# Kernel tuning notes

Measured on AMD Instinct MI355X. Metric: run time of the kernel, lower is better.

## Reference

```python
import jax, jax.numpy as jnp
import numpy as np
from jax import lax


def squash(s):
    # scale = |s|^2/(1+|s|^2); out = scale * s/|s| (eps-stabilized as in source)
    norm = jnp.sum(s * s, axis=-1, keepdims=True)
    return (norm / (1.0 + norm)) * (s / jnp.sqrt(norm + 1e-8))


def setup_inputs() -> dict:
    key = jax.random.key(0)
    k = jax.random.split(key, 4)
    B, H, C = 32, 64, 10
    x = jax.random.normal(k[0], (B, 3, H, H), jnp.float32)
    conv1_w = jax.random.normal(k[1], (256, 3, 9, 9), jnp.float32) * 0.06
    conv1_b = jnp.zeros((256,), jnp.float32)
    conv2_w = jax.random.normal(k[2], (256, 256, 9, 9), jnp.float32) * 0.02  # 256 = 8 caps * 32 routes
    conv2_b = jnp.zeros((256,), jnp.float32)
    route_w = jax.random.normal(k[3], (32, C, 8, 16), jnp.float32)  # [routes, classes, in_dim, out_dim]
    return {"x": x, "conv1_w": conv1_w, "conv1_b": conv1_b,
            "conv2_w": conv2_w, "conv2_b": conv2_b, "route_w": route_w}


def reference(x, conv1_w, conv1_b, conv2_w, conv2_b, route_w):
    dn = ("NCHW", "OIHW", "NCHW")
    # PrimaryCapsules: conv 3->256 k9 s1 + relu
    h = lax.conv_general_dilated(x, conv1_w, (1, 1), "VALID", dimension_numbers=dn)
    h = jax.nn.relu(h + conv1_b[None, :, None, None])
    # CapsuleLayer conv: 256 -> 8*32 k9 s2
    h = lax.conv_general_dilated(h, conv2_w, (2, 2), "VALID", dimension_numbers=dn)
    h = h + conv2_b[None, :, None, None]
    B, _, hh, ww = h.shape
    R, D = 32, 8  # num_routes, capsule dim
    # [B, R*D, h, w] -> [B, R, P, D], squash per capsule vector
    caps = h.reshape(B, R, D, hh, ww).transpose(0, 1, 3, 4, 2).reshape(B, R, hh * ww, D)
    caps = squash(caps)
    # DigitCapsules: per-route linear maps 8->16, shared over spatial positions
    u_hat = jnp.einsum("brpi,rcio->brpco", caps, route_w)  # [B, R, P, C, 16]
    C, O = u_hat.shape[3], u_hat.shape[4]
    u_hat = u_hat.reshape(B, R * hh * ww, C, O)  # [B, N, C, 16]
    b_log = jnp.zeros(u_hat.shape[:-1], u_hat.dtype)  # [B, N, C]
    num_routing = 3
    v = None
    for i in range(num_routing):
        c = jax.nn.softmax(b_log, axis=2)            # over classes (dim=2 in source)
        s = jnp.einsum("bnc,bnco->bco", c, u_hat)    # weighted sum over input caps
        v = squash(s)                                 # [B, C, 16]
        if i < num_routing - 1:
            b_log = b_log + jnp.einsum("bnco,bco->bnc", u_hat, v)  # agreement
    return v
```

## Files before the change

kernel.cpp:

```cpp
#include <hip/hip_runtime.h>
#include <hip/hip_bf16.h>
#include <stdint.h>

typedef __attribute__((ext_vector_type(8))) short short8;
typedef __attribute__((ext_vector_type(4))) float f32x4;
typedef unsigned int u32x4a __attribute__((vector_size(16)));
typedef unsigned int u32x4u __attribute__((vector_size(16), aligned(4)));

__device__ inline unsigned short f2bf(float f) {
    union { float f; uint32_t u; } v; v.f = f;
    uint32_t u = v.u;
    uint32_t r = (u + 0x7FFFu + ((u >> 16) & 1u)) >> 16;
    return (unsigned short)r;
}

__device__ inline void gl_lds16(const unsigned short* g, unsigned short* l) {
    __builtin_amdgcn_global_load_lds(
        (const uint32_t __attribute__((address_space(1)))*)(const void*)g,
        (uint32_t __attribute__((address_space(3)))*)(void*)l, 16, 0, 0);
}

__global__ void cvt_w1(const float* __restrict__ w, unsigned short* __restrict__ A1) {
    int idx = blockIdx.x * 256 + threadIdx.x;
    int row = idx >> 8, k = idx & 255;
    float v = (k < 243) ? w[row * 243 + k] : 0.f;
    A1[idx] = f2bf(v);
}

__global__ void cvt_w2(const float* __restrict__ w, unsigned short* __restrict__ A2t) {
    int idx = blockIdx.x * 256 + threadIdx.x;
    int j = idx & 7;
    int off16 = (idx >> 3) & 1023;
    int tile = idx >> 13;
    int tm = tile / 324, chunk = tile - tm * 324;
    int row = off16 >> 3, sw = off16 & 7;
    int koct = sw ^ (row & 7);
    int kk = chunk * 64 + koct * 8 + j;
    int oc = tm * 128 + row;
    int ic, ky, kx;
    if (kk < 18432) { ic = kk / 72; int rem = kk - ic * 72; ky = rem >> 3; kx = rem & 7; }
    else { int j2 = kk - 18432; ic = j2 / 9; ky = j2 - ic * 9; kx = 8; }
    A2t[idx] = f2bf(w[((oc * 256 + ic) * 9 + ky) * 9 + kx]);
}

__global__ __launch_bounds__(256) void conv1_gemm(
    const unsigned short* __restrict__ A,
    const float* __restrict__ x,
    const float* __restrict__ bias,
    unsigned short* __restrict__ h1)
{
    __shared__ __align__(16) unsigned short As[128 * 40];
    __shared__ __align__(16) unsigned short Bs[128 * 40];
    const int tid = threadIdx.x;
    const int m0 = blockIdx.y * 128;
    const int sx = (blockIdx.x & 7) * 98 + (blockIdx.x >> 3);
    const int n0 = sx * 128;
    const int lane = tid & 63;
    const int wave = tid >> 6;
    const int wy = wave & 1, wx = wave >> 1;
    const int l16 = lane & 15, q = lane >> 4;

    const int kp = tid & 15;
    const int gn = tid >> 4;
    int baseN[8];
#pragma unroll
    for (int j = 0; j < 8; ++j) {
        int n = n0 + gn * 8 + j;
        int b = n / 3136, p = n % 3136;
        int oy = p / 56, ox = p % 56;
        baseN[j] = b * 12288 + oy * 64 + ox;
    }

    f32x4 acc[4][4];
#pragma unroll
    for (int im = 0; im < 4; ++im)
#pragma unroll
        for (int in = 0; in < 4; ++in)
            acc[im][in] = (f32x4){0.f, 0.f, 0.f, 0.f};

    for (int k0 = 0; k0 < 256; k0 += 32) {
        __syncthreads();
#pragma unroll
        for (int s = 0; s < 2; ++s) {
            int slot = tid + s * 256;
            int row = slot >> 2, seg = slot & 3;
            u32x4a v = *(const u32x4a*)(A + (m0 + row) * 256 + k0 + seg * 8);
            *(u32x4a*)(&As[row * 40 + seg * 8]) = v;
        }
        int ka = k0 + 2 * kp, kb = ka + 1;
        int offa = 0, offb = 0;
        bool va = ka < 243, vb = kb < 243;
        if (va) { int c = ka / 81, t = ka % 81, ky = t / 9, kx = t % 9; offa = c * 4096 + ky * 64 + kx; }
        if (vb) { int c = kb / 81, t = kb % 81, ky = t / 9, kx = t % 9; offb = c * 4096 + ky * 64 + kx; }
#pragma unroll
        for (int j = 0; j < 8; ++j) {
            unsigned int ba = va ? (unsigned int)f2bf(x[baseN[j] + offa]) : 0u;
            unsigned int bb = vb ? (unsigned int)f2bf(x[baseN[j] + offb]) : 0u;
            *(unsigned int*)(&Bs[(gn * 8 + j) * 40 + 2 * kp]) = ba | (bb << 16);
        }
        __syncthreads();

        short8 af[4], bf[4];
#pragma unroll
        for (int im = 0; im < 4; ++im)
            af[im] = *(const short8*)(&As[(wy * 64 + im * 16 + l16) * 40 + q * 8]);
#pragma unroll
        for (int in = 0; in < 4; ++in)
            bf[in] = *(const short8*)(&Bs[(wx * 64 + in * 16 + l16) * 40 + q * 8]);
#pragma unroll
        for (int im = 0; im < 4; ++im)
#pragma unroll
            for (int in = 0; in < 4; ++in)
                acc[im][in] = __builtin_amdgcn_mfma_f32_16x16x32_bf16(af[im], bf[in], acc[im][in], 0, 0, 0);
    }

#pragma unroll
    for (int in = 0; in < 4; ++in) {
        int n = n0 + wx * 64 + in * 16 + l16;
        int b = n / 3136, p = n % 3136;
        int oy = p / 56, ox = p % 56;
#pragma unroll
        for (int im = 0; im < 4; ++im) {
#pragma unroll
            for (int r = 0; r < 4; ++r) {
                int oc = m0 + wy * 64 + im * 16 + q * 4 + r;
                float v = acc[im][in][r] + bias[oc];
                v = v > 0.f ? v : 0.f;
                h1[((b * 256 + oc) * 56 + oy) * 56 + ox] = f2bf(v);
            }
        }
    }
}

__global__ __launch_bounds__(256, 3) void conv2_gemm(
    const unsigned short* __restrict__ A2t,
    const unsigned short* __restrict__ h1,
    float* __restrict__ c2)
{
    __shared__ __align__(16) unsigned short As[2][8192];
    __shared__ __align__(16) unsigned short BsT[128 * 72];
    const int tid = threadIdx.x;
    const int sx = (blockIdx.x & 7) * 18 + (blockIdx.x >> 3);
    const int n0 = sx * 128;
    const int z = blockIdx.z;
    const int lane = tid & 63;
    const int wave = tid >> 6;
    const int wy = wave & 1, wx = wave >> 1;
    const int l16 = lane & 15, q = lane >> 4;

    int boff[4];
#pragma unroll
    for (int in = 0; in < 4; ++in) {
        int n = n0 + wx * 64 + in * 16 + l16;
        int b = n / 576, p = n % 576;
        int oy = p / 24, ox = p % 24;
        boff[in] = b * 802816 + (2 * oy) * 56 + 2 * ox;
    }
    const int tn = tid & 127, thalf = tid >> 7;
    int tbase;
    {
        int ng = n0 + tn;
        int b = ng / 576, p = ng % 576;
        int oy = p / 24, ox = p % 24;
        tbase = b * 802816 + (2 * oy) * 56 + 2 * ox + 8;
    }

    f32x4 acc[4][4];
#pragma unroll
    for (int im = 0; im < 4; ++im)
#pragma unroll
        for (int in = 0; in < 4; ++in)
            acc[im][in] = (f32x4){0.f, 0.f, 0.f, 0.f};

    const size_t tilebase = (size_t)blockIdx.y * 324 * 8192;

    auto issueA = [&](int c, int buf) {
        const unsigned short* at = A2t + tilebase + (size_t)c * 8192;
        int s0 = wave * 4;
#pragma unroll
        for (int i = 0; i < 4; ++i) {
            int sl = (s0 + i) * 64 + lane;
            gl_lds16(at + sl * 8, &As[buf][sl * 8]);
        }
    };
    auto loadBmain = [&](int c, short8 (&B)[2][4]) {
#pragma unroll
        for (int h = 0; h < 2; ++h) {
            int octk = c * 8 + h * 4 + q;
            int ic = octk / 9;
            int ky = octk - ic * 9;
            int off = ic * 3136 + ky * 56;
#pragma unroll
            for (int in = 0; in < 4; ++in) {
                u32x4u v = *(const u32x4u*)(h1 + boff[in] + off);
                B[h][in] = __builtin_bit_cast(short8, v);
            }
        }
    };
    auto computeChunk = [&](int buf, short8 (&B)[2][4]) {
#pragma unroll
        for (int h = 0; h < 2; ++h) {
            short8 af[4];
#pragma unroll
            for (int im = 0; im < 4; ++im) {
                int row = wy * 64 + im * 16 + l16;
                int koct = h * 4 + q;
                af[im] = *(const short8*)(&As[buf][(row * 8 + (koct ^ (row & 7))) * 8]);
            }
            __builtin_amdgcn_s_setprio(1);
#pragma unroll
            for (int im = 0; im < 4; ++im)
#pragma unroll
                for (int in = 0; in < 4; ++in)
                    acc[im][in] = __builtin_amdgcn_mfma_f32_16x16x32_bf16(
                        af[im], B[h][in], acc[im][in], 0, 0, 0);
            __builtin_amdgcn_s_setprio(0);
        }
    };

    short8 B0[2][4], B1[2][4];

    issueA(z, 0);
    loadBmain(z, B0);
    __asm__ volatile("s_waitcnt vmcnt(8)" ::: "memory");
    __builtin_amdgcn_s_barrier();
    __asm__ volatile("" ::: "memory");

    int c = z;
    for (int it = 0; it < 18; ++it) {
        issueA(c + 8, 1);
        loadBmain(c + 8, B1);
        __asm__ volatile("" ::: "memory");
        computeChunk(0, B0);
        __asm__ volatile("s_waitcnt vmcnt(8)" ::: "memory");
        __builtin_amdgcn_s_barrier();
        __asm__ volatile("" ::: "memory");

        if (it < 17) {
            issueA(c + 16, 0);
            loadBmain(c + 16, B0);
        } else {
            issueA(z + 288, 0);
        }
        __asm__ volatile("" ::: "memory");
        computeChunk(1, B1);
        __asm__ volatile("s_waitcnt vmcnt(8)" ::: "memory");
        __builtin_amdgcn_s_barrier();
        __asm__ volatile("" ::: "memory");
        c += 16;
    }

    int bt = 0;
    for (int ct = z + 288; ct < 324; ct += 8) {
        uint32_t bR[16];
        int base = ct * 64 + thalf * 32 - 18432;
#pragma unroll
        for (int p = 0; p < 16; ++p) {
            int j2 = base + 2 * p;
            int icA = j2 / 9, kyA = j2 - icA * 9;
            int icB = (j2 + 1) / 9, kyB = (j2 + 1) - icB * 9;
            uint32_t ba = h1[tbase + icA * 3136 + kyA * 56];
            uint32_t bb = h1[tbase + icB * 3136 + kyB * 56];
            bR[p] = ba | (bb << 16);
        }
        if (ct + 8 < 324) issueA(ct + 8, bt ^ 1);
        __syncthreads();
#pragma unroll
        for (int p = 0; p < 16; ++p)
            *(uint32_t*)(&BsT[tn * 72 + thalf * 32 + 2 * p]) = bR[p];
        __syncthreads();
#pragma unroll
        for (int h = 0; h < 2; ++h) {
            short8 af[4], bf[4];
#pragma unroll
            for (int im = 0; im < 4; ++im) {
                int row = wy * 64 + im * 16 + l16;
                int koct = h * 4 + q;
                af[im] = *(const short8*)(&As[bt][(row * 8 + (koct ^ (row & 7))) * 8]);
            }
#pragma unroll
            for (int in = 0; in < 4; ++in)
                bf[in] = *(const short8*)(&BsT[(wx * 64 + in * 16 + l16) * 72 + h * 32 + q * 8]);
#pragma unroll
            for (int im = 0; im < 4; ++im)
#pragma unroll
                for (int in = 0; in < 4; ++in)
                    acc[im][in] = __builtin_amdgcn_mfma_f32_16x16x32_bf16(
                        af[im], bf[in], acc[im][in], 0, 0, 0);
        }
        __syncthreads();
        bt ^= 1;
    }

    const int m0 = blockIdx.y * 128;
#pragma unroll
    for (int in = 0; in < 4; ++in) {
        int nn = n0 + wx * 64 + in * 16 + l16;
        int bb = nn / 576, pp = nn % 576;
#pragma unroll
        for (int im = 0; im < 4; ++im) {
#pragma unroll
            for (int r = 0; r < 4; ++r) {
                int oc = m0 + wy * 64 + im * 16 + q * 4 + r;
                atomicAdd(&c2[(bb * 256 + oc) * 576 + pp], acc[im][in][r]);
            }
        }
    }
}

__global__ void squash_caps(const float* __restrict__ c2, const float* __restrict__ bias,
                            float* __restrict__ caps) {
    int idx = blockIdx.x * 256 + threadIdx.x;
    int b = idx / 18432;
    int rp = idx % 18432;
    int r = rp / 576, p = rp % 576;
    float s[8]; float n2 = 0.f;
#pragma unroll
    for (int d = 0; d < 8; ++d) {
        s[d] = c2[(b * 256 + r * 8 + d) * 576 + p] + bias[r * 8 + d];
        n2 += s[d] * s[d];
    }
    float sc = (n2 / (1.f + n2)) / sqrtf(n2 + 1e-8f);
#pragma unroll
    for (int d = 0; d < 8; ++d)
        caps[idx * 8 + d] = sc * s[d];
}

__global__ __launch_bounds__(64) void capsum0(const float* __restrict__ caps,
                                              float* __restrict__ G) {
    int r = blockIdx.x, b = blockIdx.y;
    const float* cp = caps + (size_t)(b * 32 + r) * 4608;
    int tid = threadIdx.x;
    f32x4 s0 = (f32x4){0.f, 0.f, 0.f, 0.f}, s1 = s0;
    for (int jv = 0; jv < 9; ++jv) {
        const f32x4* qp = (const f32x4*)(cp + (jv * 64 + tid) * 8);
        s0 += qp[0]; s1 += qp[1];
    }
#pragma unroll
    for (int off = 32; off > 0; off >>= 1) {
#pragma unroll
        for (int k = 0; k < 4; ++k) {
            s0[k] += __shfl_down(s0[k], off, 64);
            s1[k] += __shfl_down(s1[k], off, 64);
        }
    }
    if (tid == 0) {
        float g[8] = {s0[0], s0[1], s0[2], s0[3], s1[0], s1[1], s1[2], s1[3]};
        float* gp = G + (size_t)((b * 32 + r) * 10) * 8;
        for (int cc = 0; cc < 10; ++cc)
#pragma unroll
            for (int ii = 0; ii < 8; ++ii) gp[cc * 8 + ii] = g[ii] * 0.1f;
    }
}

__global__ __launch_bounds__(64) void route_accum(const float* __restrict__ caps,
                                                  const float* __restrict__ W,
                                                  const float* __restrict__ V,
                                                  float* __restrict__ G) {
    int r = blockIdx.x, b = blockIdx.y;
    __shared__ float wv[80];
    __shared__ float red[80][64];
    int tid = threadIdx.x;
    for (int v = tid; v < 80; v += 64) {
        int cc = v >> 3, ii = v & 7;
        float s = 0.f;
#pragma unroll
        for (int o = 0; o < 16; ++o)
            s += W[((r * 10 + cc) * 8 + ii) * 16 + o] * V[(b * 10 + cc) * 16 + o];
        wv[v] = s;
    }
    __syncthreads();
    float g[80];
#pragma unroll
    for (int v = 0; v < 80; ++v) g[v] = 0.f;
    const float* cp = caps + (size_t)(b * 32 + r) * 4608;
    for (int j = 0; j < 9; ++j) {
        int p = j * 64 + tid;
        const f32x4* qp = (const f32x4*)(cp + p * 8);
        f32x4 c0 = qp[0], c1 = qp[1];
        float c8[8];
#pragma unroll
        for (int i = 0; i < 4; ++i) { c8[i] = c0[i]; c8[4 + i] = c1[i]; }
        float a[10]; float m = -1e30f;
#pragma unroll
        for (int cc = 0; cc < 10; ++cc) {
            float t = 0.f;
#pragma unroll
            for (int i = 0; i < 8; ++i) t += c8[i] * wv[cc * 8 + i];
            a[cc] = t; m = fmaxf(m, t);
        }
        float sum = 0.f;
#pragma unroll
        for (int cc = 0; cc < 10; ++cc) { a[cc] = __expf(a[cc] - m); sum += a[cc]; }
        float inv = 1.f / sum;
#pragma unroll
        for (int cc = 0; cc < 10; ++cc) {
            float w = a[cc] * inv;
#pragma unroll
            for (int i = 0; i < 8; ++i) g[cc * 8 + i] += w * c8[i];
        }
    }
#pragma unroll
    for (int v = 0; v < 80; ++v) red[v][tid] = g[v];
    __syncthreads();
    for (int v = tid; v < 80; v += 64) {
        float s = 0.f;
        for (int t = 0; t < 64; ++t) s += red[v][t];
        G[(b * 32 + r) * 80 + v] = s;
    }
}

__global__ __launch_bounds__(160) void sv_kernel(const float* __restrict__ G,
                                                 const float* __restrict__ W,
                                                 float* __restrict__ V,
                                                 float* __restrict__ out, int last) {
    int b = blockIdx.x;
    int c = threadIdx.x / 16, o = threadIdx.x % 16;
    __shared__ float sL[10][16];
    float s = 0.f;
    for (int r = 0; r < 32; ++r) {
        const float* g = G + ((b * 32 + r) * 10 + c) * 8;
        const float* w = W + ((r * 10 + c) * 8) * 16 + o;
#pragma unroll
        for (int i = 0; i < 8; ++i) s += g[i] * w[i * 16];
    }
    sL[c][o] = s;
    __syncthreads();
    float n2 = 0.f;
#pragma unroll
    for (int oo = 0; oo < 16; ++oo) { float t = sL[c][oo]; n2 += t * t; }
    float sc = (n2 / (1.f + n2)) / sqrtf(n2 + 1e-8f);
    float v = sc * s;
    V[(b * 10 + c) * 16 + o] += v;
    if (last) out[(b * 10 + c) * 16 + o] = v;
}

extern "C" void kernel_launch(void* const* d_in, const int* in_sizes, int n_in,
                              void* d_out, int out_size, void* d_ws, size_t ws_size,
                              hipStream_t stream) {
    const float* x  = (const float*)d_in[0];
    const float* w1 = (const float*)d_in[1];
    const float* b1 = (const float*)d_in[2];
    const float* w2 = (const float*)d_in[3];
    const float* b2 = (const float*)d_in[4];
    const float* rw = (const float*)d_in[5];

    char* ws = (char*)d_ws;
    unsigned short* A1   = (unsigned short*)(ws);
    unsigned short* A2   = (unsigned short*)(ws + 262144);
    unsigned short* h1   = (unsigned short*)(ws + 10878976);
    float*          c2   = (float*)(ws + 62259200);
    float*          caps = (float*)(ws + 81133568);
    float*          V    = (float*)(ws + 100007936);
    float*          G    = (float*)(ws + 100028416);

    hipLaunchKernelGGL(cvt_w1, dim3(256), dim3(256), 0, stream, w1, A1);
    hipLaunchKernelGGL(cvt_w2, dim3(20736), dim3(256), 0, stream, w2, A2);
    hipMemsetAsync(c2, 0, 18874368, stream);
    hipLaunchKernelGGL(conv1_gemm, dim3(784, 2), dim3(256), 0, stream, A1, x, b1, h1);
    hipLaunchKernelGGL(conv2_gemm, dim3(144, 2, 8), dim3(256), 0, stream, A2, h1, c2);
    hipLaunchKernelGGL(squash_caps, dim3(2304), dim3(256), 0, stream, c2, b2, caps);
    hipMemsetAsync(V, 0, 5120 * sizeof(float), stream);
    hipLaunchKernelGGL(capsum0, dim3(32, 32), dim3(64), 0, stream, caps, G);
    hipLaunchKernelGGL(sv_kernel, dim3(32), dim3(160), 0, stream, G, rw, V, (float*)d_out, 0);
    for (int it = 1; it < 3; ++it) {
        hipLaunchKernelGGL(route_accum, dim3(32, 32), dim3(64), 0, stream, caps, rw, V, G);
        hipLaunchKernelGGL(sv_kernel, dim3(32), dim3(160), 0, stream, G, rw, V,
                           (float*)d_out, it == 2 ? 1 : 0);
    }
}
```

Before: 457.1 us.

## Unify conv2 tail into main loop with triple-buffered A and direct B gathers

The conv2 GEMM's separate tail loop is removed. It staged scalar-gathered B values through an LDS transposed buffer with extra __syncthreads. The main loop now covers every chunk, and loadB falls back to per-element register gathers for the tail chunks. The A tile moves from double to triple buffering in LDS, so A prefetch runs two chunks ahead and waiting on the load counter is dropped in favour of a barrier. Swizzled A LDS offsets are also precomputed once. The change aims to remove tail synchronisation overhead and deepen the A prefetch, but the per-element tail gathers are many scalar loads and the loop trip count now depends on blockIdx.z.

Measured after the change: 725.4 us. 1.59x slower.

```diff
diff --git a/kernel.cpp b/kernel.cpp
--- a/kernel.cpp
+++ b/kernel.cpp
@@ -137,8 +137,7 @@
     const unsigned short* __restrict__ h1,
     float* __restrict__ c2)
 {
-    __shared__ __align__(16) unsigned short As[2][8192];
-    __shared__ __align__(16) unsigned short BsT[128 * 72];
+    __shared__ __align__(16) unsigned short As[3][8192];
     const int tid = threadIdx.x;
     const int sx = (blockIdx.x & 7) * 18 + (blockIdx.x >> 3);
     const int n0 = sx * 128;
@@ -156,14 +155,15 @@
         int oy = p / 24, ox = p % 24;
         boff[in] = b * 802816 + (2 * oy) * 56 + 2 * ox;
     }
-    const int tn = tid & 127, thalf = tid >> 7;
-    int tbase;
-    {
-        int ng = n0 + tn;
-        int b = ng / 576, p = ng % 576;
-        int oy = p / 24, ox = p % 24;
-        tbase = b * 802816 + (2 * oy) * 56 + 2 * ox + 8;
-    }
+    int aoff[2][4];
+#pragma unroll
+    for (int h = 0; h < 2; ++h)
+#pragma unroll
+        for (int im = 0; im < 4; ++im) {
+            int row = wy * 64 + im * 16 + l16;
+            int koct = h * 4 + q;
+            aoff[h][im] = (row * 8 + (koct ^ (row & 7))) * 8;
+        }
 
     f32x4 acc[4][4];
 #pragma unroll
@@ -173,40 +173,56 @@
             acc[im][in] = (f32x4){0.f, 0.f, 0.f, 0.f};
 
     const size_t tilebase = (size_t)blockIdx.y * 324 * 8192;
+    const int s0 = wave * 4;
 
     auto issueA = [&](int c, int buf) {
         const unsigned short* at = A2t + tilebase + (size_t)c * 8192;
-        int s0 = wave * 4;
 #pragma unroll
         for (int i = 0; i < 4; ++i) {
             int sl = (s0 + i) * 64 + lane;
             gl_lds16(at + sl * 8, &As[buf][sl * 8]);
         }
     };
-    auto loadBmain = [&](int c, short8 (&B)[2][4]) {
-#pragma unroll
-        for (int h = 0; h < 2; ++h) {
-            int octk = c * 8 + h * 4 + q;
-            int ic = octk / 9;
-            int ky = octk - ic * 9;
-            int off = ic * 3136 + ky * 56;
-#pragma unroll
-            for (int in = 0; in < 4; ++in) {
-                u32x4u v = *(const u32x4u*)(h1 + boff[in] + off);
-                B[h][in] = __builtin_bit_cast(short8, v);
+    auto loadB = [&](int c, short8 (&B)[2][4]) {
+        if (c < 288) {
+#pragma unroll
+            for (int h = 0; h < 2; ++h) {
+                int octk = c * 8 + h * 4 + q;
+                int ic = octk / 9;
+                int ky = octk - ic * 9;
+                int off = ic * 3136 + ky * 56;
+#pragma unroll
+                for (int in = 0; in < 4; ++in) {
+                    u32x4u v = *(const u32x4u*)(h1 + boff[in] + off);
+                    B[h][in] = __builtin_bit_cast(short8, v);
+                }
+            }
+        } else {
+#pragma unroll
+            for (int h = 0; h < 2; ++h) {
+                int kbase = c * 64 + (h * 4 + q) * 8 - 18432;
+#pragma unroll
+                for (int in = 0; in < 4; ++in) {
+                    short8 v;
+#pragma unroll
+                    for (int j = 0; j < 8; ++j) {
+                        int j2 = kbase + j;
+                        int ic = j2 / 9, ky = j2 - ic * 9;
+                        v[j] = (short)h1[boff[in] + 8 + ic * 3136 + ky * 56];
+                    }
+                    B[h][in] = v;
+                }
             }
         }
     };
     auto computeChunk = [&](int buf, short8 (&B)[2][4]) {
+        const unsigned short* ab = &As[buf][0];
 #pragma unroll
         for (int h = 0; h < 2; ++h) {
             short8 af[4];
 #pragma unroll
-            for (int im = 0; im < 4; ++im) {
-                int row = wy * 64 + im * 16 + l16;
-                int koct = h * 4 + q;
-                af[im] = *(const short8*)(&As[buf][(row * 8 + (koct ^ (row & 7))) * 8]);
-            }
+            for (int im = 0; im < 4; ++im)
+                af[im] = *(const short8*)(ab + aoff[h][im]);
             __builtin_amdgcn_s_setprio(1);
 #pragma unroll
             for (int im = 0; im < 4; ++im)
@@ -219,77 +235,42 @@
     };
 
     short8 B0[2][4], B1[2][4];
+    const int nch = (324 - z + 7) >> 3;
 
     issueA(z, 0);
-    loadBmain(z, B0);
+    issueA(z + 8, 1);
+    __asm__ volatile("" ::: "memory");
+    loadB(z, B0);
     __asm__ volatile("s_waitcnt vmcnt(8)" ::: "memory");
     __builtin_amdgcn_s_barrier();
     __asm__ volatile("" ::: "memory");
 
     int c = z;
-    for (int it = 0; it < 18; ++it) {
-        issueA(c + 8, 1);
-        loadBmain(c + 8, B1);
-        __asm__ volatile("" ::: "memory");
-        computeChunk(0, B0);
-        __asm__ volatile("s_waitcnt vmcnt(8)" ::: "memory");
+    int bufA = 0;
+    const int half = nch >> 1;
+    for (int it = 0; it < half; ++it) {
+        const int i0 = 2 * it;
+        if (i0 + 2 < nch) { int bn = bufA + 2; if (bn >= 3) bn -= 3; issueA(c + 16, bn); }
+        __asm__ volatile("" ::: "memory");
+        if (i0 + 1 < nch) loadB(c + 8, B1);
+        computeChunk(bufA, B0);
+        if (++bufA == 3) bufA = 0;
+        __asm__ volatile("" ::: "memory");
         __builtin_amdgcn_s_barrier();
         __asm__ volatile("" ::: "memory");
-
-        if (it < 17) {
-            issueA(c + 16, 0);
-            loadBmain(c + 16, B0);
-        } else {
-            issueA(z + 288, 0);
-        }
-        __asm__ volatile("" ::: "memory");
-        computeChunk(1, B1);
-        __asm__ volatile("s_waitcnt vmcnt(8)" ::: "memory");
+        c += 8;
+        if (i0 + 3 < nch) { int bn = bufA + 2; if (bn >= 3) bn -= 3; issueA(c + 16, bn); }
+        __asm__ volatile("" ::: "memory");
+        if (i0 + 2 < nch) loadB(c + 8, B0);
+        computeChunk(bufA, B1);
+        if (++bufA == 3) bufA = 0;
+        __asm__ volatile("" ::: "memory");
         __builtin_amdgcn_s_barrier();
         __asm__ volatile("" ::: "memory");
-        c += 16;
-    }
-
-    int bt = 0;
-    for (int ct = z + 288; ct < 324; ct += 8) {
-        uint32_t bR[16];
-        int base = ct * 64 + thalf * 32 - 18432;
-#pragma unroll
-        for (int p = 0; p < 16; ++p) {
-            int j2 = base + 2 * p;
-            int icA = j2 / 9, kyA = j2 - icA * 9;
-            int icB = (j2 + 1) / 9, kyB = (j2 + 1) - icB * 9;
-            uint32_t ba = h1[tbase + icA * 3136 + kyA * 56];
-            uint32_t bb = h1[tbase + icB * 3136 + kyB * 56];
-            bR[p] = ba | (bb << 16);
-        }
-        if (ct + 8 < 324) issueA(ct + 8, bt ^ 1);
-        __syncthreads();
-#pragma unroll
-        for (int p = 0; p < 16; ++p)
-            *(uint32_t*)(&BsT[tn * 72 + thalf * 32 + 2 * p]) = bR[p];
-        __syncthreads();
-#pragma unroll
-        for (int h = 0; h < 2; ++h) {
-            short8 af[4], bf[4];
-#pragma unroll
-            for (int im = 0; im < 4; ++im) {
-                int row = wy * 64 + im * 16 + l16;
-                int koct = h * 4 + q;
-                af[im] = *(const short8*)(&As[bt][(row * 8 + (koct ^ (row & 7))) * 8]);
-            }
-#pragma unroll
-            for (int in = 0; in < 4; ++in)
-                bf[in] = *(const short8*)(&BsT[(wx * 64 + in * 16 + l16) * 72 + h * 32 + q * 8]);
-#pragma unroll
-            for (int im = 0; im < 4; ++im)
-#pragma unroll
-                for (int in = 0; in < 4; ++in)
-                    acc[im][in] = __builtin_amdgcn_mfma_f32_16x16x32_bf16(
-                        af[im], bf[in], acc[im][in], 0, 0, 0);
-        }
-        __syncthreads();
-        bt ^= 1;
+        c += 8;
+    }
+    if (nch & 1) {
+        computeChunk(bufA, B0);
     }
 
     const int m0 = blockIdx.y * 128;
```

## Triple-buffer conv2 A tiles in LDS and reuse a buffer for the tail

Applied to the files above, without the earlier changes.

The main K loop of the conv2 GEMM moves from a double-buffered to a triple-buffered LDS scheme for the weight tiles. The async global-to-LDS copy is issued two chunks ahead while the activation fragments are prefetched one chunk ahead. The loop is unrolled so buffer indices are compile-time constants, and the explicit vmcnt waits give way to implicit ordering through the register-consumed B loads. The separate transposed B tile for the tail loop is dropped and stored, swizzled, into the third A buffer, which keeps LDS use about the same. Precomputed LDS fragment offsets remove per-iteration address math. The risk is that the changed wait/barrier placement could expose load latency, or LDS hazards if the compiler inserts conservative waits.

Result: slower. 476.3 us (+4.2%).

```diff
diff --git a/kernel.cpp b/kernel.cpp
--- a/kernel.cpp
+++ b/kernel.cpp
@@ -137,8 +137,7 @@
     const unsigned short* __restrict__ h1,
     float* __restrict__ c2)
 {
-    __shared__ __align__(16) unsigned short As[2][8192];
-    __shared__ __align__(16) unsigned short BsT[128 * 72];
+    __shared__ __align__(16) unsigned short As[3][8192];
     const int tid = threadIdx.x;
     const int sx = (blockIdx.x & 7) * 18 + (blockIdx.x >> 3);
     const int n0 = sx * 128;
@@ -156,6 +155,108 @@
         int oy = p / 24, ox = p % 24;
         boff[in] = b * 802816 + (2 * oy) * 56 + 2 * ox;
     }
+    int aoff[2][4];
+#pragma unroll
+    for (int h = 0; h < 2; ++h)
+#pragma unroll
+        for (int im = 0; im < 4; ++im) {
+            int row = wy * 64 + im * 16 + l16;
+            int koct = h * 4 + q;
+            aoff[h][im] = (row * 8 + (koct ^ (row & 7))) * 8;
+        }
+
+    f32x4 acc[4][4];
+#pragma unroll
+    for (int im = 0; im < 4; ++im)
+#pragma unroll
+        for (int in = 0; in < 4; ++in)
+            acc[im][in] = (f32x4){0.f, 0.f, 0.f, 0.f};
+
+    const size_t tilebase = (size_t)blockIdx.y * 324 * 8192;
+    const int s0 = wave * 4;
+
+    auto issueA = [&](int c, int buf) {
+        const unsigned short* at = A2t + tilebase + (size_t)c * 8192;
+#pragma unroll
+        for (int i = 0; i < 4; ++i) {
+            int sl = (s0 + i) * 64 + lane;
+            gl_lds16(at + sl * 8, &As[buf][sl * 8]);
+        }
+    };
+    auto loadB = [&](int c, short8 (&B)[2][4]) {
+#pragma unroll
+        for (int h = 0; h < 2; ++h) {
+            int octk = c * 8 + h * 4 + q;
+            int ic = octk / 9;
+            int ky = octk - ic * 9;
+            int off = ic * 3136 + ky * 56;
+#pragma unroll
+            for (int in = 0; in < 4; ++in) {
+                u32x4u v = *(const u32x4u*)(h1 + boff[in] + off);
+                B[h][in] = __builtin_bit_cast(short8, v);
+            }
+        }
+    };
+    auto computeChunk = [&](int buf, short8 (&B)[2][4]) {
+        const unsigned short* ab = &As[buf][0];
+#pragma unroll
+        for (int h = 0; h < 2; ++h) {
+            short8 af[4];
+#pragma unroll
+            for (int im = 0; im < 4; ++im)
+                af[im] = *(const short8*)(ab + aoff[h][im]);
+            __builtin_amdgcn_s_setprio(1);
+#pragma unroll
+            for (int im = 0; im < 4; ++im)
+#pragma unroll
+                for (int in = 0; in < 4; ++in)
+                    acc[im][in] = __builtin_amdgcn_mfma_f32_16x16x32_bf16(
+                        af[im], B[h][in], acc[im][in], 0, 0, 0);
+            __builtin_amdgcn_s_setprio(0);
+        }
+    };
+
+    short8 B0[2][4], B1[2][4];
+
+    issueA(z, 0);
+    issueA(z + 8, 1);
+    __asm__ volatile("" ::: "memory");
+    loadB(z, B0);
+    __asm__ volatile("s_waitcnt vmcnt(8)" ::: "memory");
+    __builtin_amdgcn_s_barrier();
+    __asm__ volatile("" ::: "memory");
+
+#define HALF(i, bufc, bufn, Bc, Bn, doIssue, doLoadB)                     \
+    do {                                                                  \
+        if (doIssue) issueA(z + 8 * ((i) + 2), (bufn));                   \
+        __asm__ volatile("" ::: "memory");                                \
+        if (doLoadB) loadB(z + 8 * ((i) + 1), (Bn));                      \
+        computeChunk((bufc), (Bc));                                       \
+        __asm__ volatile("" ::: "memory");                                \
+        __builtin_amdgcn_s_barrier();                                     \
+        __asm__ volatile("" ::: "memory");                                \
+    } while (0)
+
+#pragma unroll 1
+    for (int j = 0; j < 5; ++j) {
+        int i = 6 * j;
+        HALF(i + 0, 0, 2, B0, B1, true, true);
+        HALF(i + 1, 1, 0, B1, B0, true, true);
+        HALF(i + 2, 2, 1, B0, B1, true, true);
+        HALF(i + 3, 0, 2, B1, B0, true, true);
+        HALF(i + 4, 1, 0, B0, B1, true, true);
+        HALF(i + 5, 2, 1, B1, B0, true, true);
+    }
+    HALF(30, 0, 2, B0, B1, true, true);
+    HALF(31, 1, 0, B1, B0, true, true);
+    HALF(32, 2, 1, B0, B1, true, true);
+    HALF(33, 0, 2, B1, B0, true, true);
+    HALF(34, 1, 0, B0, B1, false, true);
+    HALF(35, 2, 1, B1, B0, false, false);
+#undef HALF
+
+    issueA(z + 288, 0);
+
     const int tn = tid & 127, thalf = tid >> 7;
     int tbase;
     {
@@ -164,91 +265,14 @@
         int oy = p / 24, ox = p % 24;
         tbase = b * 802816 + (2 * oy) * 56 + 2 * ox + 8;
     }
-
-    f32x4 acc[4][4];
-#pragma unroll
-    for (int im = 0; im < 4; ++im)
-#pragma unroll
-        for (int in = 0; in < 4; ++in)
-            acc[im][in] = (f32x4){0.f, 0.f, 0.f, 0.f};
-
-    const size_t tilebase = (size_t)blockIdx.y * 324 * 8192;
-
-    auto issueA = [&](int c, int buf) {
-        const unsigned short* at = A2t + tilebase + (size_t)c * 8192;
-        int s0 = wave * 4;
-#pragma unroll
-        for (int i = 0; i < 4; ++i) {
-            int sl = (s0 + i) * 64 + lane;
-            gl_lds16(at + sl * 8, &As[buf][sl * 8]);
-        }
-    };
-    auto loadBmain = [&](int c, short8 (&B)[2][4]) {
-#pragma unroll
-        for (int h = 0; h < 2; ++h) {
-            int octk = c * 8 + h * 4 + q;
-            int ic = octk / 9;
-            int ky = octk - ic * 9;
-            int off = ic * 3136 + ky * 56;
-#pragma unroll
-            for (int in = 0; in < 4; ++in) {
-                u32x4u v = *(const u32x4u*)(h1 + boff[in] + off);
-                B[h][in] = __builtin_bit_cast(short8, v);
-            }
-        }
-    };
-    auto computeChunk = [&](int buf, short8 (&B)[2][4]) {
-#pragma unroll
-        for (int h = 0; h < 2; ++h) {
-            short8 af[4];
-#pragma unroll
-            for (int im = 0; im < 4; ++im) {
-                int row = wy * 64 + im * 16 + l16;
-                int koct = h * 4 + q;
-                af[im] = *(const short8*)(&As[buf][(row * 8 + (koct ^ (row & 7))) * 8]);
-            }
-            __builtin_amdgcn_s_setprio(1);
-#pragma unroll
-            for (int im = 0; im < 4; ++im)
-#pragma unroll
-                for (int in = 0; in < 4; ++in)
-                    acc[im][in] = __builtin_amdgcn_mfma_f32_16x16x32_bf16(
-                        af[im], B[h][in], acc[im][in], 0, 0, 0);
-            __builtin_amdgcn_s_setprio(0);
-        }
-    };
-
-    short8 B0[2][4], B1[2][4];
-
-    issueA(z, 0);
-    loadBmain(z, B0);
-    __asm__ volatile("s_waitcnt vmcnt(8)" ::: "memory");
-    __builtin_amdgcn_s_barrier();
-    __asm__ volatile("" ::: "memory");
-
-    int c = z;
-    for (int it = 0; it < 18; ++it) {
-        issueA(c + 8, 1);
-        loadBmain(c + 8, B1);
-        __asm__ volatile("" ::: "memory");
-        computeChunk(0, B0);
-        __asm__ volatile("s_waitcnt vmcnt(8)" ::: "memory");
-        __builtin_amdgcn_s_barrier();
-        __asm__ volatile("" ::: "memory");
-
-        if (it < 17) {
-            issueA(c + 16, 0);
-            loadBmain(c + 16, B0);
-        } else {
-            issueA(z + 288, 0);
-        }
-        __asm__ volatile("" ::: "memory");
-        computeChunk(1, B1);
-        __asm__ volatile("s_waitcnt vmcnt(8)" ::: "memory");
-        __builtin_amdgcn_s_barrier();
-        __asm__ volatile("" ::: "memory");
-        c += 16;
-    }
+    int boffT[2][4];
+#pragma unroll
+    for (int h = 0; h < 2; ++h)
+#pragma unroll
+        for (int in = 0; in < 4; ++in) {
+            int row = wx * 64 + in * 16 + l16;
+            boffT[h][in] = (row * 8 + ((h * 4 + q) ^ (row & 7))) * 8;
+        }
 
     int bt = 0;
     for (int ct = z + 288; ct < 324; ct += 8) {
@@ -265,22 +289,25 @@
         }
         if (ct + 8 < 324) issueA(ct + 8, bt ^ 1);
         __syncthreads();
-#pragma unroll
-        for (int p = 0; p < 16; ++p)
-            *(uint32_t*)(&BsT[tn * 72 + thalf * 32 + 2 * p]) = bR[p];
+        {
+            int rsw = tn * 8, rx = tn & 7;
+#pragma unroll
+            for (int p = 0; p < 16; ++p) {
+                int col = thalf * 32 + 2 * p;
+                int a16 = (rsw + ((col >> 3) ^ rx)) * 8 + (col & 7);
+                *(uint32_t*)(&As[2][a16]) = bR[p];
+            }
+        }
         __syncthreads();
 #pragma unroll
         for (int h = 0; h < 2; ++h) {
             short8 af[4], bf[4];
 #pragma unroll
-            for (int im = 0; im < 4; ++im) {
-                int row = wy * 64 + im * 16 + l16;
-                int koct = h * 4 + q;
-                af[im] = *(const short8*)(&As[bt][(row * 8 + (koct ^ (row & 7))) * 8]);
-            }
+            for (int im = 0; im < 4; ++im)
+                af[im] = *(const short8*)(&As[bt][aoff[h][im]]);
 #pragma unroll
             for (int in = 0; in < 4; ++in)
-                bf[in] = *(const short8*)(&BsT[(wx * 64 + in * 16 + l16) * 72 + h * 32 + q * 8]);
+                bf[in] = *(const short8*)(&As[2][boffT[h][in]]);
 #pragma unroll
             for (int im = 0; im < 4; ++im)
 #pragma unroll
```

## Split A-operand sourcing between LDS and direct global loads; swizzle BsT

Applied to the files above, without the earlier changes.

In conv2_gemm, only the top 64 rows of each A tile are now staged into LDS. Waves with wy==1 read their A fragments straight from global memory (relying on cache hits), which halves the LDS A buffer. The tail-path BsT tile switches from a padded 72-stride layout to an XOR-swizzled 64-stride layout, so total shared memory drops and occupancy may rise. The risk is that the direct global A reads for half the waves add memory latency to the MFMA critical path. Their wait counts can also force the compiler to drain the prefetched B loads early, weakening the software pipeline.

Result: slower. 619.1 us (+35.4%).

```diff
diff --git a/kernel.cpp b/kernel.cpp
--- a/kernel.cpp
+++ b/kernel.cpp
@@ -137,8 +137,8 @@
     const unsigned short* __restrict__ h1,
     float* __restrict__ c2)
 {
-    __shared__ __align__(16) unsigned short As[2][8192];
-    __shared__ __align__(16) unsigned short BsT[128 * 72];
+    __shared__ __align__(16) unsigned short As[2][4096];
+    __shared__ __align__(16) unsigned short BsT[8192];
     const int tid = threadIdx.x;
     const int sx = (blockIdx.x & 7) * 18 + (blockIdx.x >> 3);
     const int n0 = sx * 128;
@@ -156,6 +156,100 @@
         int oy = p / 24, ox = p % 24;
         boff[in] = b * 802816 + (2 * oy) * 56 + 2 * ox;
     }
+    const int sw0 = (0 * 4 + q) ^ (l16 & 7);
+    const int sw1 = (1 * 4 + q) ^ (l16 & 7);
+
+    f32x4 acc[4][4];
+#pragma unroll
+    for (int im = 0; im < 4; ++im)
+#pragma unroll
+        for (int in = 0; in < 4; ++in)
+            acc[im][in] = (f32x4){0.f, 0.f, 0.f, 0.f};
+
+    const size_t tilebase = (size_t)blockIdx.y * 324 * 8192;
+
+    auto issueA = [&](int c, int buf) {
+        const unsigned short* at = A2t + tilebase + (size_t)c * 8192;
+#pragma unroll
+        for (int i = 0; i < 2; ++i) {
+            int sl = (wave * 2 + i) * 64 + lane;
+            gl_lds16(at + sl * 8, &As[buf][sl * 8]);
+        }
+    };
+    auto loadB = [&](int c, short8 (&B)[2][4]) {
+#pragma unroll
+        for (int h = 0; h < 2; ++h) {
+            int octk = c * 8 + h * 4 + q;
+            int ic = octk / 9;
+            int ky = octk - ic * 9;
+            int off = ic * 3136 + ky * 56;
+#pragma unroll
+            for (int in = 0; in < 4; ++in) {
+                u32x4u v = *(const u32x4u*)(h1 + boff[in] + off);
+                B[h][in] = __builtin_bit_cast(short8, v);
+            }
+        }
+    };
+    auto computeChunk = [&](int buf, short8 (&B)[2][4], const unsigned short* at) {
+#pragma unroll
+        for (int h = 0; h < 2; ++h) {
+            const int swh = h ? sw1 : sw0;
+            short8 af[4];
+            if (wy == 0) {
+                const unsigned short* ab = &As[buf][l16 * 64 + swh * 8];
+#pragma unroll
+                for (int im = 0; im < 4; ++im)
+                    af[im] = *(const short8*)(ab + im * 1024);
+            } else {
+                const unsigned short* ag = at + (64 + l16) * 64 + swh * 8;
+#pragma unroll
+                for (int im = 0; im < 4; ++im)
+                    af[im] = *(const short8*)(ag + im * 1024);
+            }
+            __builtin_amdgcn_s_setprio(1);
+#pragma unroll
+            for (int im = 0; im < 4; ++im)
+#pragma unroll
+                for (int in = 0; in < 4; ++in)
+                    acc[im][in] = __builtin_amdgcn_mfma_f32_16x16x32_bf16(
+                        af[im], B[h][in], acc[im][in], 0, 0, 0);
+            __builtin_amdgcn_s_setprio(0);
+        }
+    };
+
+    short8 B0[2][4], B1[2][4];
+
+    issueA(z, 0);
+    loadB(z, B0);
+    __asm__ volatile("s_waitcnt vmcnt(8)" ::: "memory");
+    __builtin_amdgcn_s_barrier();
+    __asm__ volatile("" ::: "memory");
+
+    int c = z;
+    for (int it = 0; it < 18; ++it) {
+        const unsigned short* at0 = A2t + tilebase + (size_t)c * 8192;
+        issueA(c + 8, 1);
+        loadB(c + 8, B1);
+        __asm__ volatile("" ::: "memory");
+        computeChunk(0, B0, at0);
+        __asm__ volatile("s_waitcnt vmcnt(8)" ::: "memory");
+        __builtin_amdgcn_s_barrier();
+        __asm__ volatile("" ::: "memory");
+
+        if (it < 17) {
+            issueA(c + 16, 0);
+            loadB(c + 16, B0);
+        } else {
+            issueA(z + 288, 0);
+        }
+        __asm__ volatile("" ::: "memory");
+        computeChunk(1, B1, at0 + 8 * 8192);
+        __asm__ volatile("s_waitcnt vmcnt(8)" ::: "memory");
+        __builtin_amdgcn_s_barrier();
+        __asm__ volatile("" ::: "memory");
+        c += 16;
+    }
+
     const int tn = tid & 127, thalf = tid >> 7;
     int tbase;
     {
@@ -164,91 +258,14 @@
         int oy = p / 24, ox = p % 24;
         tbase = b * 802816 + (2 * oy) * 56 + 2 * ox + 8;
     }
-
-    f32x4 acc[4][4];
-#pragma unroll
-    for (int im = 0; im < 4; ++im)
-#pragma unroll
-        for (int in = 0; in < 4; ++in)
-            acc[im][in] = (f32x4){0.f, 0.f, 0.f, 0.f};
-
-    const size_t tilebase = (size_t)blockIdx.y * 324 * 8192;
-
-    auto issueA = [&](int c, int buf) {
-        const unsigned short* at = A2t + tilebase + (size_t)c * 8192;
-        int s0 = wave * 4;
-#pragma unroll
-        for (int i = 0; i < 4; ++i) {
-            int sl = (s0 + i) * 64 + lane;
-            gl_lds16(at + sl * 8, &As[buf][sl * 8]);
-        }
-    };
-    auto loadBmain = [&](int c, short8 (&B)[2][4]) {
-#pragma unroll
-        for (int h = 0; h < 2; ++h) {
-            int octk = c * 8 + h * 4 + q;
-            int ic = octk / 9;
-            int ky = octk - ic * 9;
-            int off = ic * 3136 + ky * 56;
-#pragma unroll
-            for (int in = 0; in < 4; ++in) {
-                u32x4u v = *(const u32x4u*)(h1 + boff[in] + off);
-                B[h][in] = __builtin_bit_cast(short8, v);
-            }
-        }
-    };
-    auto computeChunk = [&](int buf, short8 (&B)[2][4]) {
-#pragma unroll
-        for (int h = 0; h < 2; ++h) {
-            short8 af[4];
-#pragma unroll
-            for (int im = 0; im < 4; ++im) {
-                int row = wy * 64 + im * 16 + l16;
-                int koct = h * 4 + q;
-                af[im] = *(const short8*)(&As[buf][(row * 8 + (koct ^ (row & 7))) * 8]);
-            }
-            __builtin_amdgcn_s_setprio(1);
-#pragma unroll
-            for (int im = 0; im < 4; ++im)
-#pragma unroll
-                for (int in = 0; in < 4; ++in)
-                    acc[im][in] = __builtin_amdgcn_mfma_f32_16x16x32_bf16(
-                        af[im], B[h][in], acc[im][in], 0, 0, 0);
-            __builtin_amdgcn_s_setprio(0);
-        }
-    };
-
-    short8 B0[2][4], B1[2][4];
-
-    issueA(z, 0);
-    loadBmain(z, B0);
-    __asm__ volatile("s_waitcnt vmcnt(8)" ::: "memory");
-    __builtin_amdgcn_s_barrier();
-    __asm__ volatile("" ::: "memory");
-
-    int c = z;
-    for (int it = 0; it < 18; ++it) {
-        issueA(c + 8, 1);
-        loadBmain(c + 8, B1);
-        __asm__ volatile("" ::: "memory");
-        computeChunk(0, B0);
-        __asm__ volatile("s_waitcnt vmcnt(8)" ::: "memory");
-        __builtin_amdgcn_s_barrier();
-        __asm__ volatile("" ::: "memory");
-
-        if (it < 17) {
-            issueA(c + 16, 0);
-            loadBmain(c + 16, B0);
-        } else {
-            issueA(z + 288, 0);
-        }
-        __asm__ volatile("" ::: "memory");
-        computeChunk(1, B1);
-        __asm__ volatile("s_waitcnt vmcnt(8)" ::: "memory");
-        __builtin_amdgcn_s_barrier();
-        __asm__ volatile("" ::: "memory");
-        c += 16;
-    }
+    int boffT[2][4];
+#pragma unroll
+    for (int h = 0; h < 2; ++h)
+#pragma unroll
+        for (int in = 0; in < 4; ++in) {
+            int row = wx * 64 + in * 16 + l16;
+            boffT[h][in] = (row * 8 + ((h * 4 + q) ^ (row & 7))) * 8;
+        }
 
     int bt = 0;
     for (int ct = z + 288; ct < 324; ct += 8) {
@@ -265,22 +282,35 @@
         }
         if (ct + 8 < 324) issueA(ct + 8, bt ^ 1);
         __syncthreads();
-#pragma unroll
-        for (int p = 0; p < 16; ++p)
-            *(uint32_t*)(&BsT[tn * 72 + thalf * 32 + 2 * p]) = bR[p];
+        {
+            int rsw = tn * 8, rx = tn & 7;
+#pragma unroll
+            for (int p = 0; p < 16; ++p) {
+                int col = thalf * 32 + 2 * p;
+                int a16 = (rsw + ((col >> 3) ^ rx)) * 8 + (col & 7);
+                *(uint32_t*)(&BsT[a16]) = bR[p];
+            }
+        }
         __syncthreads();
+        const unsigned short* atT = A2t + tilebase + (size_t)ct * 8192;
 #pragma unroll
         for (int h = 0; h < 2; ++h) {
+            const int swh = h ? sw1 : sw0;
             short8 af[4], bf[4];
-#pragma unroll
-            for (int im = 0; im < 4; ++im) {
-                int row = wy * 64 + im * 16 + l16;
-                int koct = h * 4 + q;
-                af[im] = *(const short8*)(&As[bt][(row * 8 + (koct ^ (row & 7))) * 8]);
+            if (wy == 0) {
+                const unsigned short* ab = &As[bt][l16 * 64 + swh * 8];
+#pragma unroll
+                for (int im = 0; im < 4; ++im)
+                    af[im] = *(const short8*)(ab + im * 1024);
+            } else {
+                const unsigned short* ag = atT + (64 + l16) * 64 + swh * 8;
+#pragma unroll
+                for (int im = 0; im < 4; ++im)
+                    af[im] = *(const short8*)(ag + im * 1024);
             }
 #pragma unroll
             for (int in = 0; in < 4; ++in)
-                bf[in] = *(const short8*)(&BsT[(wx * 64 + in * 16 + l16) * 72 + h * 32 + q * 8]);
+                bf[in] = *(const short8*)(&BsT[boffT[h][in]]);
 #pragma unroll
             for (int im = 0; im < 4; ++im)
 #pragma unroll
```
